# Performance work log

Hardware: AMD Instinct MI355X
Metric: run time of the kernel (lower is better)

## Reference

```python
import jax, jax.numpy as jnp
import numpy as np

N, E = 20000, 320000
CUR, HID, OUT, H = 256, 256, 64, 6  # cur_dim, hidden_dim, output_dim, gat heads


def setup_inputs() -> dict:
    key = jax.random.key(0)
    ks = jax.random.split(key, 16)
    p = lambda k, shape: jax.random.normal(k, shape, jnp.float32) * 0.05
    return dict(
        x=jax.random.normal(ks[0], (N, CUR), jnp.float32),
        edge_index=jax.random.randint(ks[1], (2, E), 0, N),
        edge_weight=jax.random.uniform(ks[2], (E,), jnp.float32),
        Wp=p(ks[3], (CUR, HID)), bp=p(ks[4], (HID,)),
        W_gat=p(ks[5], (HID, H * OUT)),
        att_src=p(ks[6], (H, OUT)), att_dst=p(ks[7], (H, OUT)),
        b_gat=p(ks[8], (H * OUT,)),
        W_gcn0=p(ks[9], (HID, OUT)), b_gcn0=p(ks[10], (OUT,)),
        W_gcn1=p(ks[11], (HID, OUT)), b_gcn1=p(ks[12], (OUT,)),
        W_arma_init=p(ks[13], (H * OUT, OUT)),
        W_arma_root=p(ks[14], (H * OUT, OUT)),
        b_arma=p(ks[15], (OUT,)),
    )


def _seg_sum(v, ids, n):
    return jax.ops.segment_sum(v, ids, num_segments=n)


def _gat(h, src, dst, W, a_s, a_d, b):
    # PyG GATConv: add self loops, per-edge attention, softmax over incoming edges.
    n = h.shape[0]
    loops = jnp.arange(n)
    s = jnp.concatenate([src, loops])
    d = jnp.concatenate([dst, loops])
    xw = (h @ W).reshape(n, H, OUT)               # [N,H,F]
    al = (xw * a_s).sum(-1)                       # [N,H] source term
    ar = (xw * a_d).sum(-1)                       # [N,H] target term
    e = jax.nn.leaky_relu(al[s] + ar[d], 0.2)     # [E',H]
    m = jax.ops.segment_max(e, d, num_segments=n)  # stable softmax per target
    pe = jnp.exp(e - m[d])
    alpha = pe / _seg_sum(pe, d, n)[d]
    out = _seg_sum(alpha[:, :, None] * xw[s], d, n)  # [N,H,F]
    return out.reshape(n, H * OUT) + b


def _gcn(h, src, dst, w, W, b):
    # PyG GCNConv: self loops (weight 1), symmetric D^-1/2 A D^-1/2 normalization.
    n = h.shape[0]
    loops = jnp.arange(n)
    s = jnp.concatenate([src, loops])
    d = jnp.concatenate([dst, loops])
    w2 = jnp.concatenate([w, jnp.ones((n,), h.dtype)])
    deg = _seg_sum(w2, d, n)
    dinv = jnp.where(deg > 0, jax.lax.rsqrt(deg), 0.0)
    norm = dinv[s] * w2 * dinv[d]
    xw = h @ W
    return _seg_sum(norm[:, None] * xw[s], d, n) + b


def _arma(h, src, dst, w, Wi, Wr, b):
    # PyG ARMAConv, num_stacks=1, num_layers=1, act=ReLU; gcn_norm WITHOUT self loops.
    n = h.shape[0]
    deg = _seg_sum(w, dst, n)
    dinv = jnp.where(deg > 0, jax.lax.rsqrt(deg), 0.0)
    norm = dinv[src] * w * dinv[dst]
    t = h @ Wi
    agg = _seg_sum(norm[:, None] * t[src], dst, n)
    return jax.nn.relu(agg + h @ Wr + b)


def reference(x, edge_index, edge_weight, Wp, bp, W_gat, att_src, att_dst, b_gat,
              W_gcn0, b_gcn0, W_gcn1, b_gcn1, W_arma_init, W_arma_root, b_arma):
    src, dst = edge_index[0], edge_index[1]
    h = x @ Wp + bp
    lrelu = lambda v: jax.nn.leaky_relu(v, 0.01)  # F.leaky_relu default slope
    h1 = lrelu(_gat(h, src, dst, W_gat, att_src, att_dst, b_gat))   # [N, 6*64]
    h2 = lrelu(_gcn(h, src, dst, edge_weight, W_gcn0, b_gcn0))       # [N, 64]
    h3 = lrelu(_gcn(h, src, dst, edge_weight, W_gcn1, b_gcn1))       # [N, 64]
    h4 = lrelu(_arma(h1, src, dst, edge_weight, W_arma_init, W_arma_root, b_arma))
    return jnp.tanh(jnp.concatenate([h1, h2, h3, h4], axis=1))      # [N, 576]
```

## Files before the change

### kernel.cpp

```cpp
#include <hip/hip_runtime.h>


#define NN 20000
#define EE 320000
#define GATD 384
#define NH 6
#define OUTD 64
#define ODIM 576

typedef __bf16 bf16_8 __attribute__((ext_vector_type(8)));
typedef float f32_4 __attribute__((ext_vector_type(4)));

__device__ __forceinline__ float lrelu(float x, float s) { return x > 0.f ? x : s * x; }

__device__ __forceinline__ float loadf(const void* p, size_t i, int f32) {
  return f32 ? ((const float*)p)[i] : (float)((const __bf16*)p)[i];
}

struct ProbeArgs {
  const void* ptr[15];
  int cnt[15];
  int flagidx[15];
  const int* ei;
};
__global__ void k_probe_all(ProbeArgs a, int* __restrict__ flags) {
  __shared__ int cnt;
  if (threadIdx.x == 0) cnt = 0;
  __syncthreads();
  int b = blockIdx.x;
  if (b < 15) {
    const unsigned short* u = (const unsigned short*)a.ptr[b];
    int m = a.cnt[b] < 2048 ? a.cnt[b] : 2048;
    int c = 0;
    for (int i = threadIdx.x; i < m; i += 256) {
      float v = __uint_as_float(((unsigned int)u[i]) << 16);
      if (!(fabsf(v) < 1e4f)) c++;
    }
    if (c) atomicAdd(&cnt, c);
    __syncthreads();
    if (threadIdx.x == 0) flags[a.flagidx[b]] = (cnt > m / 16) ? 1 : 0;
  } else {
    int c = 0;
    for (int i = threadIdx.x; i < 1024; i += 256)
      if (a.ei[2 * i + 1] != 0) c++;
    if (c) atomicAdd(&cnt, c);
    __syncthreads();
    if (threadIdx.x == 0) flags[16] = (cnt <= 2) ? 1 : 0;
  }
}

struct CvtSeg { const void* in; __bf16* out; int n; int flagidx; int blk0; };
struct CvtArgs { CvtSeg s[7]; };
__global__ void k_cvt_all(CvtArgs a, const int* __restrict__ flags) {
  int b = blockIdx.x;
  int k = 0;
  while (k + 1 < 7 && a.s[k + 1].blk0 <= b) k++;
  const CvtSeg sg = a.s[k];
  int i = (b - sg.blk0) * 256 + threadIdx.x;
  if (i >= sg.n) return;
  sg.out[i] = flags[sg.flagidx] ? (__bf16)((const float*)sg.in)[i] : ((const __bf16*)sg.in)[i];
}

struct TSeg { const void* in; __bf16* out; int R; int C; int flagidx; int blk0; };
struct TArgs { TSeg s[6]; };
__global__ void k_cvt_t_all(TArgs a, const int* __restrict__ flags) {
  __shared__ float t[32][33];
  int b = blockIdx.x;
  int k = 0;
  while (k + 1 < 6 && a.s[k + 1].blk0 <= b) k++;
  const TSeg sg = a.s[k];
  int f32 = flags[sg.flagidx];
  int tpx = (sg.C + 31) >> 5;
  int lt = b - sg.blk0;
  int c0 = (lt % tpx) * 32, r0 = (lt / tpx) * 32;
  int tid = threadIdx.x;
  for (int idx = tid; idx < 1024; idx += 256) {
    int r = idx >> 5, c = idx & 31;
    if (r0 + r < sg.R && c0 + c < sg.C)
      t[r][c] = loadf(sg.in, (size_t)(r0 + r) * sg.C + (c0 + c), f32);
  }
  __syncthreads();
  for (int idx = tid; idx < 1024; idx += 256) {
    int r = idx >> 5, c = idx & 31;
    if (c0 + r < sg.C && r0 + c < sg.R)
      sg.out[(size_t)(c0 + r) * sg.R + (r0 + c)] = (__bf16)t[c][r];
  }
}

__global__ void k_count(const int* __restrict__ ei, const void* __restrict__ ew,
                        const int* __restrict__ flags,
                        int* __restrict__ deg, float* __restrict__ wdeg) {
  int e = blockIdx.x * 256 + threadIdx.x;
  if (e >= EE) return;
  int sh = flags[16];
  int d = ei[(size_t)(EE + e) << sh];
  atomicAdd(&deg[d], 1);
  atomicAdd(&wdeg[d], loadf(ew, e, flags[2]));
}

__global__ void k_scan(const int* __restrict__ deg, int* __restrict__ rowstart) {
  __shared__ int ps[256];
  int t = threadIdx.x;
  const int per = (NN + 255) / 256;
  int lo = t * per, hi = min(NN, lo + per);
  if (lo > NN) lo = NN;
  int s = 0;
  for (int i = lo; i < hi; i++) s += deg[i];
  ps[t] = s;
  __syncthreads();
  if (t == 0) { int a = 0; for (int i = 0; i < 256; i++) { int v = ps[i]; ps[i] = a; a += v; } }
  __syncthreads();
  int a = ps[t];
  for (int i = lo; i < hi; i++) { rowstart[i] = a; a += deg[i]; }
  if (t == 255) rowstart[NN] = a;
}

__global__ void k_fill(const int* __restrict__ ei, const void* __restrict__ ew,
                       const int* __restrict__ flags, const int* __restrict__ rowstart,
                       int* __restrict__ cursor,
                       int* __restrict__ csr_src, float* __restrict__ csr_w) {
  int e = blockIdx.x * 256 + threadIdx.x;
  if (e >= EE) return;
  int sh = flags[16];
  int d = ei[(size_t)(EE + e) << sh];
  int s = ei[(size_t)e << sh];
  int pos = rowstart[d] + atomicAdd(&cursor[d], 1);
  csr_src[pos] = s;
  csr_w[pos] = loadf(ew, e, flags[2]);
}

__global__ void k_dinv(const float* __restrict__ wdeg, float* __restrict__ dg, float* __restrict__ da) {
  int i = blockIdx.x * 256 + threadIdx.x;
  if (i >= NN) return;
  float w = wdeg[i];
  dg[i] = rsqrtf(w + 1.0f);
  da[i] = w > 0.f ? rsqrtf(w) : 0.f;
}

template<bool HAS_BIAS>
__global__ __launch_bounds__(256) void gemm64(const void* __restrict__ A,
    const int* __restrict__ aflag, const __bf16* __restrict__ Bt,
    const __bf16* __restrict__ bias, __bf16* __restrict__ Cout,
    int M, int N, int K, int ldc) {
  __shared__ __bf16 Al[64][40];
  __shared__ __bf16 Bl[64][40];
  int a32 = *aflag;
  int tid = threadIdx.x;
  int w = tid >> 6, lane = tid & 63;
  int quad = lane >> 4, r = lane & 15;
  int row0 = blockIdx.x * 64, col0 = blockIdx.y * 64;
  f32_4 acc[4] = {};
  int srow = tid >> 2;
  int koff = (tid & 3) * 8;
  for (int kt = 0; kt < K; kt += 32) {
    int arow = row0 + srow;
    if (a32) {
      float4 a0 = {0.f, 0.f, 0.f, 0.f}, a1 = {0.f, 0.f, 0.f, 0.f};
      if (arow < M) {
        const float* ap = (const float*)A + (size_t)arow * K + kt + koff;
        a0 = *(const float4*)ap;
        a1 = *(const float4*)(ap + 4);
      }
      bf16_8 t;
      t[0] = (__bf16)a0.x; t[1] = (__bf16)a0.y; t[2] = (__bf16)a0.z; t[3] = (__bf16)a0.w;
      t[4] = (__bf16)a1.x; t[5] = (__bf16)a1.y; t[6] = (__bf16)a1.z; t[7] = (__bf16)a1.w;
      *(bf16_8*)(&Al[srow][koff]) = t;
    } else {
      float4 av = {0.f, 0.f, 0.f, 0.f};
      if (arow < M) av = *(const float4*)((const __bf16*)A + (size_t)arow * K + kt + koff);
      *(float4*)(&Al[srow][koff]) = av;
    }
    float4 bv = *(const float4*)(Bt + (size_t)(col0 + srow) * K + kt + koff);
    *(float4*)(&Bl[srow][koff]) = bv;
    __syncthreads();
    bf16_8 bfrag = *(const bf16_8*)(&Bl[w * 16 + r][quad * 8]);
#pragma unroll
    for (int mt = 0; mt < 4; mt++) {
      bf16_8 afrag = *(const bf16_8*)(&Al[mt * 16 + r][quad * 8]);
      acc[mt] = __builtin_amdgcn_mfma_f32_16x16x32_bf16(afrag, bfrag, acc[mt], 0, 0, 0);
    }
    __syncthreads();
  }
  int ccol = col0 + w * 16 + r;
  float bv = HAS_BIAS ? (float)bias[ccol] : 0.0f;
#pragma unroll
  for (int mt = 0; mt < 4; mt++) {
#pragma unroll
    for (int rr = 0; rr < 4; rr++) {
      int crow = row0 + mt * 16 + quad * 4 + rr;
      if (crow < M) Cout[(size_t)crow * ldc + ccol] = (__bf16)(acc[mt][rr] + bv);
    }
  }
}

__global__ void k_alar_w(const __bf16* __restrict__ xwb, const __bf16* __restrict__ as_,
                         const __bf16* __restrict__ ad_,
                         float* __restrict__ al, float* __restrict__ ar) {
  int p = blockIdx.x * 4 + (threadIdx.x >> 6);
  int lane = threadIdx.x & 63;
  if (p >= NN * NH) return;
  int i = p / NH, h = p - i * NH;
  float xv = (float)xwb[(size_t)i * GATD + h * OUTD + lane];
  float s1 = xv * (float)as_[h * OUTD + lane];
  float s2 = xv * (float)ad_[h * OUTD + lane];
  for (int off = 32; off; off >>= 1) { s1 += __shfl_xor(s1, off); s2 += __shfl_xor(s2, off); }
  if (lane == 0) { al[p] = s1; ar[p] = s2; }
}

__global__ __launch_bounds__(256) void k_gat2(const __bf16* __restrict__ xwb,
    const float* __restrict__ al, const float* __restrict__ ar,
    const int* __restrict__ rowstart, const int* __restrict__ csr_src,
    const __bf16* __restrict__ bgat,
    __bf16* __restrict__ h1b, float* __restrict__ out) {
  int wv = threadIdx.x >> 6, lane = threadIdx.x & 63;
  int i = blockIdx.x * 4 + wv;
  __shared__ int   src_sh[4][64];
  __shared__ float ex_sh[4][64][NH];
  __shared__ int   mc_sh[4];
  int e0 = rowstart[i], e1 = rowstart[i + 1];
  if (lane == 0) mc_sh[wv] = (e1 - e0 + 63) >> 6;
  float arv[NH], exs[NH], acc[NH], denp[NH];
#pragma unroll
  for (int h = 0; h < NH; h++) arv[h] = ar[i * NH + h];
#pragma unroll
  for (int h = 0; h < NH; h++) {
    float e = lrelu(al[i * NH + h] + arv[h], 0.2f);
    exs[h] = __expf(e);
    acc[h] = exs[h] * (float)xwb[(size_t)i * GATD + h * OUTD + lane];
    denp[h] = 0.f;
  }
  __syncthreads();
  int mch = max(max(mc_sh[0], mc_sh[1]), max(mc_sh[2], mc_sh[3]));
  for (int c = 0; c < mch; c++) {
    if (c) __syncthreads();
    int base = e0 + c * 64;
    int cnt = e1 - base; cnt = cnt < 0 ? 0 : (cnt > 64 ? 64 : cnt);
    if (lane < cnt) {
      int s = csr_src[base + lane];
      src_sh[wv][lane] = s;
#pragma unroll
      for (int h = 0; h < NH; h++) {
        float ex = __expf(lrelu(al[s * NH + h] + arv[h], 0.2f));
        ex_sh[wv][lane][h] = ex;
        denp[h] += ex;
      }
    }
    __syncthreads();
    int j = 0;
    for (; j + 2 <= cnt; j += 2) {
      int s0 = src_sh[wv][j], s1 = src_sh[wv][j + 1];
      const __bf16* r0 = xwb + (size_t)s0 * GATD + lane;
      const __bf16* r1 = xwb + (size_t)s1 * GATD + lane;
      float x0[NH], x1[NH];
#pragma unroll
      for (int h = 0; h < NH; h++) { x0[h] = (float)r0[h * OUTD]; x1[h] = (float)r1[h * OUTD]; }
#pragma unroll
      for (int h = 0; h < NH; h++)
        acc[h] += ex_sh[wv][j][h] * x0[h] + ex_sh[wv][j + 1][h] * x1[h];
    }
    if (j < cnt) {
      int s0 = src_sh[wv][j];
      const __bf16* r0 = xwb + (size_t)s0 * GATD + lane;
#pragma unroll
      for (int h = 0; h < NH; h++) acc[h] += ex_sh[wv][j][h] * (float)r0[h * OUTD];
    }
  }
#pragma unroll
  for (int h = 0; h < NH; h++) {
    float d = denp[h];
    for (int off = 32; off; off >>= 1) d += __shfl_xor(d, off);
    d += exs[h];
    float v = acc[h] / d + (float)bgat[h * OUTD + lane];
    v = lrelu(v, 0.01f);
    h1b[(size_t)i * GATD + h * OUTD + lane] = (__bf16)v;
    out[(size_t)i * ODIM + h * OUTD + lane] = tanhf(v);
  }
}

__global__ __launch_bounds__(256) void k_gcnarma2(const __bf16* __restrict__ xwgb,
    const __bf16* __restrict__ trb, const int* __restrict__ rowstart,
    const int* __restrict__ csr_src, const float* __restrict__ csr_w,
    const float* __restrict__ dgcn, const float* __restrict__ darma,
    const __bf16* __restrict__ b0, const __bf16* __restrict__ b1,
    const __bf16* __restrict__ ba, float* __restrict__ out) {
  int wv = threadIdx.x >> 6, lane = threadIdx.x & 63;
  int i = blockIdx.x * 4 + wv;
  __shared__ int   src_sh[4][64];
  __shared__ float wg_sh[4][64], wa_sh[4][64];
  __shared__ int   mc_sh[4];
  int e0 = rowstart[i], e1 = rowstart[i + 1];
  if (lane == 0) mc_sh[wv] = (e1 - e0 + 63) >> 6;
  __syncthreads();
  int mch = max(max(mc_sh[0], mc_sh[1]), max(mc_sh[2], mc_sh[3]));
  float g0 = 0.f, g1 = 0.f, aa = 0.f;
  for (int c = 0; c < mch; c++) {
    if (c) __syncthreads();
    int base = e0 + c * 64;
    int cnt = e1 - base; cnt = cnt < 0 ? 0 : (cnt > 64 ? 64 : cnt);
    if (lane < cnt) {
      int eidx = base + lane;
      int s = csr_src[eidx];
      float wvv = csr_w[eidx];
      src_sh[wv][lane] = s;
      wg_sh[wv][lane] = dgcn[s] * wvv;
      wa_sh[wv][lane] = darma[s] * wvv;
    }
    __syncthreads();
    int j = 0;
    for (; j + 2 <= cnt; j += 2) {
      int s0 = src_sh[wv][j], s1 = src_sh[wv][j + 1];
      float wg0 = wg_sh[wv][j], wg1 = wg_sh[wv][j + 1];
      float wa0 = wa_sh[wv][j], wa1 = wa_sh[wv][j + 1];
      const __bf16* p0 = xwgb + (size_t)s0 * 128;
      const __bf16* p1 = xwgb + (size_t)s1 * 128;
      const __bf16* q0 = trb + (size_t)s0 * 128;
      const __bf16* q1 = trb + (size_t)s1 * 128;
      g0 += wg0 * (float)p0[lane] + wg1 * (float)p1[lane];
      g1 += wg0 * (float)p0[lane + 64] + wg1 * (float)p1[lane + 64];
      aa += wa0 * (float)q0[lane] + wa1 * (float)q1[lane];
    }
    if (j < cnt) {
      int s0 = src_sh[wv][j];
      float wg0 = wg_sh[wv][j], wa0 = wa_sh[wv][j];
      const __bf16* p0 = xwgb + (size_t)s0 * 128;
      const __bf16* q0 = trb + (size_t)s0 * 128;
      g0 += wg0 * (float)p0[lane];
      g1 += wg0 * (float)p0[lane + 64];
      aa += wa0 * (float)q0[lane];
    }
  }
  float di = dgcn[i];
  float v0 = lrelu(di * g0 + di * di * (float)xwgb[(size_t)i * 128 + lane] + (float)b0[lane], 0.01f);
  float v1 = lrelu(di * g1 + di * di * (float)xwgb[(size_t)i * 128 + 64 + lane] + (float)b1[lane], 0.01f);
  out[(size_t)i * ODIM + 384 + lane] = tanhf(v0);
  out[(size_t)i * ODIM + 448 + lane] = tanhf(v1);
  float va = darma[i] * aa + (float)trb[(size_t)i * 128 + 64 + lane] + (float)ba[lane];
  va = fmaxf(va, 0.f);
  out[(size_t)i * ODIM + 512 + lane] = tanhf(va);
}

extern "C" void kernel_launch(void* const* d_in, const int* in_sizes, int n_in,
                              void* d_out, int out_size, void* d_ws, size_t ws_size,
                              hipStream_t stream) {
  const int* ei = (const int*)d_in[1];
  float* out = (float*)d_out;

  char* ws = (char*)d_ws;
  size_t off = 0;
  auto alloc = [&](size_t bytes) -> void* {
    void* p = ws + off;
    off += (bytes + 255) & ~(size_t)255;
    return p;
  };
  int*    flags    = (int*)alloc(32 * 4);
  int*    deg      = (int*)alloc((size_t)3 * NN * 4);
  int*    cursor   = deg + NN;
  float*  wdeg     = (float*)(deg + 2 * NN);
  int*    rowstart = (int*)alloc((size_t)(NN + 1) * 4);
  int*    csr_src  = (int*)alloc((size_t)EE * 4);
  float*  csr_w    = (float*)alloc((size_t)EE * 4);
  float*  dgcn     = (float*)alloc((size_t)NN * 4);
  float*  darma    = (float*)alloc((size_t)NN * 4);
  float*  al       = (float*)alloc((size_t)NN * NH * 4);
  float*  ar       = (float*)alloc((size_t)NN * NH * 4);
  __bf16* bpb   = (__bf16*)alloc(256 * 2);
  __bf16* asb   = (__bf16*)alloc(384 * 2);
  __bf16* adb   = (__bf16*)alloc(384 * 2);
  __bf16* bgatb = (__bf16*)alloc(384 * 2);
  __bf16* bg0b  = (__bf16*)alloc(64 * 2);
  __bf16* bg1b  = (__bf16*)alloc(64 * 2);
  __bf16* bab   = (__bf16*)alloc(64 * 2);
  __bf16* Wp_t    = (__bf16*)alloc(256 * 256 * 2);
  __bf16* Wgat_t  = (__bf16*)alloc(384 * 256 * 2);
  __bf16* Wg01_t  = (__bf16*)alloc(128 * 256 * 2);
  __bf16* Warma_t = (__bf16*)alloc(128 * 384 * 2);
  char* regA = (char*)alloc((size_t)NN * GATD * 2);
  __bf16* h   = (__bf16*)regA;
  __bf16* h1b = (__bf16*)regA;
  char* regB = (char*)alloc((size_t)NN * GATD * 2);
  __bf16* xwb = (__bf16*)regB;
  __bf16* trb = (__bf16*)regB;
  __bf16* xwgb = (__bf16*)alloc((size_t)NN * 128 * 2);
  (void)ws_size; (void)in_sizes; (void)n_in; (void)out_size;

  hipMemsetAsync(ws, 0, 256 + (size_t)3 * NN * 4, stream);

  dim3 tb(256);
  ProbeArgs pa;
  const int pidx[15] = {0, 2, 3, 4, 5, 6, 7, 8, 9, 10, 11, 12, 13, 14, 15};
  const int pcnt[15] = {NN * 256, EE, 256 * 256, 256, 256 * 384, NH * OUTD, NH * OUTD,
                        NH * OUTD, 256 * 64, 64, 256 * 64, 64, GATD * OUTD, GATD * OUTD, 64};
  for (int k = 0; k < 15; k++) { pa.ptr[k] = d_in[pidx[k]]; pa.cnt[k] = pcnt[k]; pa.flagidx[k] = pidx[k]; }
  pa.ei = ei;
  k_probe_all<<<dim3(16), tb, 0, stream>>>(pa, flags);

  CvtArgs ca;
  {
    struct { int idx; __bf16* out; int n; } cv[7] = {
      {4, bpb, 256}, {6, asb, 384}, {7, adb, 384}, {8, bgatb, 384},
      {10, bg0b, 64}, {12, bg1b, 64}, {15, bab, 64},
    };
    int blk = 0;
    for (int k = 0; k < 7; k++) {
      ca.s[k].in = d_in[cv[k].idx]; ca.s[k].out = cv[k].out; ca.s[k].n = cv[k].n;
      ca.s[k].flagidx = cv[k].idx; ca.s[k].blk0 = blk;
      blk += (cv[k].n + 255) / 256;
    }
    k_cvt_all<<<dim3(blk), tb, 0, stream>>>(ca, flags);
  }

  TArgs ta;
  {
    struct { int idx; __bf16* out; int R; int C; } tv[6] = {
      {3,  Wp_t,             256, 256},
      {5,  Wgat_t,           256, 384},
      {9,  Wg01_t,           256, 64},
      {11, Wg01_t + 64 * 256, 256, 64},
      {13, Warma_t,          384, 64},
      {14, Warma_t + 64 * 384, 384, 64},
    };
    int blk = 0;
    for (int k = 0; k < 6; k++) {
      ta.s[k].in = d_in[tv[k].idx]; ta.s[k].out = tv[k].out;
      ta.s[k].R = tv[k].R; ta.s[k].C = tv[k].C;
      ta.s[k].flagidx = tv[k].idx; ta.s[k].blk0 = blk;
      blk += ((tv[k].R + 31) / 32) * ((tv[k].C + 31) / 32);
    }
    k_cvt_t_all<<<dim3(blk), tb, 0, stream>>>(ta, flags);
  }

  k_count<<<dim3((EE + 255) / 256), tb, 0, stream>>>(ei, d_in[2], flags, deg, wdeg);
  k_scan<<<dim3(1), tb, 0, stream>>>(deg, rowstart);
  k_fill<<<dim3((EE + 255) / 256), tb, 0, stream>>>(ei, d_in[2], flags, rowstart, cursor, csr_src, csr_w);
  k_dinv<<<dim3((NN + 255) / 256), tb, 0, stream>>>(wdeg, dgcn, darma);

  const int MB64 = (NN + 63) / 64;
  gemm64<true ><<<dim3(MB64, 4), tb, 0, stream>>>(d_in[0], &flags[0], Wp_t, bpb, h, NN, 256, 256, 256);
  gemm64<false><<<dim3(MB64, 6), tb, 0, stream>>>(h, &flags[30], Wgat_t, nullptr, xwb, NN, 384, 256, 384);
  k_alar_w<<<dim3((NN * NH + 3) / 4), tb, 0, stream>>>(xwb, asb, adb, al, ar);
  gemm64<false><<<dim3(MB64, 2), tb, 0, stream>>>(h, &flags[30], Wg01_t, nullptr, xwgb, NN, 128, 256, 128);
  k_gat2<<<dim3(NN / 4), tb, 0, stream>>>(xwb, al, ar, rowstart, csr_src, bgatb, h1b, out);
  gemm64<false><<<dim3(MB64, 2), tb, 0, stream>>>(h1b, &flags[30], Warma_t, nullptr, trb, NN, 128, 384, 128);
  k_gcnarma2<<<dim3(NN / 4), tb, 0, stream>>>(xwgb, trb, rowstart, csr_src, csr_w,
                                              dgcn, darma, bg0b, bg1b, bab, out);
}
```

Baseline: 342.6 us.

## Interleave head features in GEMM output and fuse GAT/GCN projection GEMMs

```diff
diff --git a/kernel.cpp b/kernel.cpp
--- a/kernel.cpp
+++ b/kernel.cpp
@@ -11,7 +11,11 @@
 typedef __bf16 bf16_8 __attribute__((ext_vector_type(8)));
 typedef float f32_4 __attribute__((ext_vector_type(4)));
 
+struct u96 { unsigned x, y, z; };
+
 __device__ __forceinline__ float lrelu(float x, float s) { return x > 0.f ? x : s * x; }
+__device__ __forceinline__ float bflo(unsigned p) { return __uint_as_float(p << 16); }
+__device__ __forceinline__ float bfhi(unsigned p) { return __uint_as_float(p & 0xffff0000u); }
 
 __device__ __forceinline__ float loadf(const void* p, size_t i, int f32) {
   return f32 ? ((const float*)p)[i] : (float)((const __bf16*)p)[i];
@@ -98,19 +102,26 @@
   atomicAdd(&wdeg[d], loadf(ew, e, flags[2]));
 }
 
-__global__ void k_scan(const int* __restrict__ deg, int* __restrict__ rowstart) {
-  __shared__ int ps[256];
+__global__ __launch_bounds__(256) void k_scan(const int* __restrict__ deg, int* __restrict__ rowstart) {
+  __shared__ int wsum[4];
   int t = threadIdx.x;
   const int per = (NN + 255) / 256;
-  int lo = t * per, hi = min(NN, lo + per);
-  if (lo > NN) lo = NN;
+  int lo = t * per; if (lo > NN) lo = NN;
+  int hi = lo + per; if (hi > NN) hi = NN;
   int s = 0;
   for (int i = lo; i < hi; i++) s += deg[i];
-  ps[t] = s;
+  int lane = t & 63, wv = t >> 6;
+  int run = s;
+  for (int off = 1; off < 64; off <<= 1) {
+    int u = __shfl_up(run, off);
+    if (lane >= off) run += u;
+  }
+  if (lane == 63) wsum[wv] = run;
   __syncthreads();
-  if (t == 0) { int a = 0; for (int i = 0; i < 256; i++) { int v = ps[i]; ps[i] = a; a += v; } }
-  __syncthreads();
-  int a = ps[t];
+  int wbase = 0;
+#pragma unroll
+  for (int w = 0; w < 4; w++) { int v = wsum[w]; if (w < wv) wbase += v; }
+  int a = wbase + run - s;
   for (int i = lo; i < hi; i++) { rowstart[i] = a; a += deg[i]; }
   if (t == 255) rowstart[NN] = a;
 }
@@ -140,8 +151,10 @@
 template<bool HAS_BIAS>
 __global__ __launch_bounds__(256) void gemm64(const void* __restrict__ A,
     const int* __restrict__ aflag, const __bf16* __restrict__ Bt,
-    const __bf16* __restrict__ bias, __bf16* __restrict__ Cout,
-    int M, int N, int K, int ldc) {
+    const __bf16* __restrict__ bias,
+    __bf16* __restrict__ C1, int n1, int ldc1, int P1,
+    __bf16* __restrict__ C2, int ldc2, int P2,
+    int M, int K) {
   __shared__ __bf16 Al[64][40];
   __shared__ __bf16 Bl[64][40];
   int a32 = *aflag;
@@ -181,33 +194,40 @@
     }
     __syncthreads();
   }
-  int ccol = col0 + w * 16 + r;
-  float bv = HAS_BIAS ? (float)bias[ccol] : 0.0f;
+  int ccg = col0 + w * 16 + r;
+  __bf16* Cp; int ldc; int ccol; int P;
+  if (col0 < n1) { Cp = C1; ldc = ldc1; ccol = ccg; P = P1; }
+  else           { Cp = C2; ldc = ldc2; ccol = ccg - n1; P = P2; }
+  int cc = (P > 1) ? ((ccol & 63) * P + (ccol >> 6)) : ccol;
+  float bv = HAS_BIAS ? (float)bias[ccg] : 0.0f;
 #pragma unroll
   for (int mt = 0; mt < 4; mt++) {
 #pragma unroll
     for (int rr = 0; rr < 4; rr++) {
       int crow = row0 + mt * 16 + quad * 4 + rr;
-      if (crow < M) Cout[(size_t)crow * ldc + ccol] = (__bf16)(acc[mt][rr] + bv);
-    }
-  }
-}
-
-__global__ void k_alar_w(const __bf16* __restrict__ xwb, const __bf16* __restrict__ as_,
+      if (crow < M) Cp[(size_t)crow * ldc + cc] = (__bf16)(acc[mt][rr] + bv);
+    }
+  }
+}
+
+__global__ void k_alar_w(const __bf16* __restrict__ xwp, const __bf16* __restrict__ as_,
                          const __bf16* __restrict__ ad_,
                          float* __restrict__ al, float* __restrict__ ar) {
-  int p = blockIdx.x * 4 + (threadIdx.x >> 6);
+  int i = blockIdx.x * 4 + (threadIdx.x >> 6);
   int lane = threadIdx.x & 63;
-  if (p >= NN * NH) return;
-  int i = p / NH, h = p - i * NH;
-  float xv = (float)xwb[(size_t)i * GATD + h * OUTD + lane];
-  float s1 = xv * (float)as_[h * OUTD + lane];
-  float s2 = xv * (float)ad_[h * OUTD + lane];
-  for (int off = 32; off; off >>= 1) { s1 += __shfl_xor(s1, off); s2 += __shfl_xor(s2, off); }
-  if (lane == 0) { al[p] = s1; ar[p] = s2; }
-}
-
-__global__ __launch_bounds__(256) void k_gat2(const __bf16* __restrict__ xwb,
+  if (i >= NN) return;
+  u96 u = *(const u96*)(xwp + (size_t)i * GATD + lane * 6);
+  float v[NH] = {bflo(u.x), bfhi(u.x), bflo(u.y), bfhi(u.y), bflo(u.z), bfhi(u.z)};
+#pragma unroll
+  for (int h = 0; h < NH; h++) {
+    float s1 = v[h] * (float)as_[h * OUTD + lane];
+    float s2 = v[h] * (float)ad_[h * OUTD + lane];
+    for (int off = 32; off; off >>= 1) { s1 += __shfl_xor(s1, off); s2 += __shfl_xor(s2, off); }
+    if (lane == 0) { al[i * NH + h] = s1; ar[i * NH + h] = s2; }
+  }
+}
+
+__global__ __launch_bounds__(256) void k_gat2(const __bf16* __restrict__ xwp,
     const float* __restrict__ al, const float* __restrict__ ar,
     const int* __restrict__ rowstart, const int* __restrict__ csr_src,
     const __bf16* __restrict__ bgat,
@@ -215,18 +235,20 @@
   int wv = threadIdx.x >> 6, lane = threadIdx.x & 63;
   int i = blockIdx.x * 4 + wv;
   __shared__ int   src_sh[4][64];
-  __shared__ float ex_sh[4][64][NH];
+  __shared__ __attribute__((aligned(16))) float ex_sh[4][64][NH];
   __shared__ int   mc_sh[4];
   int e0 = rowstart[i], e1 = rowstart[i + 1];
   if (lane == 0) mc_sh[wv] = (e1 - e0 + 63) >> 6;
   float arv[NH], exs[NH], acc[NH], denp[NH];
 #pragma unroll
   for (int h = 0; h < NH; h++) arv[h] = ar[i * NH + h];
+  u96 us = *(const u96*)(xwp + (size_t)i * GATD + lane * 6);
+  float sv[NH] = {bflo(us.x), bfhi(us.x), bflo(us.y), bfhi(us.y), bflo(us.z), bfhi(us.z)};
 #pragma unroll
   for (int h = 0; h < NH; h++) {
     float e = lrelu(al[i * NH + h] + arv[h], 0.2f);
     exs[h] = __expf(e);
-    acc[h] = exs[h] * (float)xwb[(size_t)i * GATD + h * OUTD + lane];
+    acc[h] = exs[h] * sv[h];
     denp[h] = 0.f;
   }
   __syncthreads();
@@ -248,21 +270,31 @@
     __syncthreads();
     int j = 0;
     for (; j + 2 <= cnt; j += 2) {
-      int s0 = src_sh[wv][j], s1 = src_sh[wv][j + 1];
-      const __bf16* r0 = xwb + (size_t)s0 * GATD + lane;
-      const __bf16* r1 = xwb + (size_t)s1 * GATD + lane;
-      float x0[NH], x1[NH];
-#pragma unroll
-      for (int h = 0; h < NH; h++) { x0[h] = (float)r0[h * OUTD]; x1[h] = (float)r1[h * OUTD]; }
-#pragma unroll
-      for (int h = 0; h < NH; h++)
-        acc[h] += ex_sh[wv][j][h] * x0[h] + ex_sh[wv][j + 1][h] * x1[h];
+      int2 ss = *(const int2*)&src_sh[wv][j];
+      u96 u0 = *(const u96*)(xwp + (size_t)ss.x * GATD + lane * 6);
+      u96 u1 = *(const u96*)(xwp + (size_t)ss.y * GATD + lane * 6);
+      const float2* ep0 = (const float2*)ex_sh[wv][j];
+      const float2* ep1 = (const float2*)ex_sh[wv][j + 1];
+      float2 ea0 = ep0[0], eb0 = ep0[1], ec0 = ep0[2];
+      float2 ea1 = ep1[0], eb1 = ep1[1], ec1 = ep1[2];
+      acc[0] += ea0.x * bflo(u0.x) + ea1.x * bflo(u1.x);
+      acc[1] += ea0.y * bfhi(u0.x) + ea1.y * bfhi(u1.x);
+      acc[2] += eb0.x * bflo(u0.y) + eb1.x * bflo(u1.y);
+      acc[3] += eb0.y * bfhi(u0.y) + eb1.y * bfhi(u1.y);
+      acc[4] += ec0.x * bflo(u0.z) + ec1.x * bflo(u1.z);
+      acc[5] += ec0.y * bfhi(u0.z) + ec1.y * bfhi(u1.z);
     }
     if (j < cnt) {
       int s0 = src_sh[wv][j];
-      const __bf16* r0 = xwb + (size_t)s0 * GATD + lane;
-#pragma unroll
-      for (int h = 0; h < NH; h++) acc[h] += ex_sh[wv][j][h] * (float)r0[h * OUTD];
+      u96 u0 = *(const u96*)(xwp + (size_t)s0 * GATD + lane * 6);
+      const float2* ep0 = (const float2*)ex_sh[wv][j];
+      float2 ea0 = ep0[0], eb0 = ep0[1], ec0 = ep0[2];
+      acc[0] += ea0.x * bflo(u0.x);
+      acc[1] += ea0.y * bfhi(u0.x);
+      acc[2] += eb0.x * bflo(u0.y);
+      acc[3] += eb0.y * bfhi(u0.y);
+      acc[4] += ec0.x * bflo(u0.z);
+      acc[5] += ec0.y * bfhi(u0.z);
     }
   }
 #pragma unroll
@@ -277,7 +309,7 @@
   }
 }
 
-__global__ __launch_bounds__(256) void k_gcnarma2(const __bf16* __restrict__ xwgb,
+__global__ __launch_bounds__(256) void k_gcnarma2(const __bf16* __restrict__ xwgp,
     const __bf16* __restrict__ trb, const int* __restrict__ rowstart,
     const int* __restrict__ csr_src, const float* __restrict__ csr_w,
     const float* __restrict__ dgcn, const float* __restrict__ darma,
@@ -286,7 +318,7 @@
   int wv = threadIdx.x >> 6, lane = threadIdx.x & 63;
   int i = blockIdx.x * 4 + wv;
   __shared__ int   src_sh[4][64];
-  __shared__ float wg_sh[4][64], wa_sh[4][64];
+  __shared__ __attribute__((aligned(16))) float wg_sh[4][64], wa_sh[4][64];
   __shared__ int   mc_sh[4];
   int e0 = rowstart[i], e1 = rowstart[i + 1];
   if (lane == 0) mc_sh[wv] = (e1 - e0 + 63) >> 6;
@@ -308,30 +340,31 @@
     __syncthreads();
     int j = 0;
     for (; j + 2 <= cnt; j += 2) {
-      int s0 = src_sh[wv][j], s1 = src_sh[wv][j + 1];
-      float wg0 = wg_sh[wv][j], wg1 = wg_sh[wv][j + 1];
-      float wa0 = wa_sh[wv][j], wa1 = wa_sh[wv][j + 1];
-      const __bf16* p0 = xwgb + (size_t)s0 * 128;
-      const __bf16* p1 = xwgb + (size_t)s1 * 128;
-      const __bf16* q0 = trb + (size_t)s0 * 128;
-      const __bf16* q1 = trb + (size_t)s1 * 128;
-      g0 += wg0 * (float)p0[lane] + wg1 * (float)p1[lane];
-      g1 += wg0 * (float)p0[lane + 64] + wg1 * (float)p1[lane + 64];
-      aa += wa0 * (float)q0[lane] + wa1 * (float)q1[lane];
+      int2 ss = *(const int2*)&src_sh[wv][j];
+      float2 wg = *(const float2*)&wg_sh[wv][j];
+      float2 wa = *(const float2*)&wa_sh[wv][j];
+      unsigned x0 = *(const unsigned*)(xwgp + (size_t)ss.x * 128 + lane * 2);
+      unsigned x1 = *(const unsigned*)(xwgp + (size_t)ss.y * 128 + lane * 2);
+      float t0 = (float)trb[(size_t)ss.x * 128 + lane];
+      float t1 = (float)trb[(size_t)ss.y * 128 + lane];
+      g0 += wg.x * bflo(x0) + wg.y * bflo(x1);
+      g1 += wg.x * bfhi(x0) + wg.y * bfhi(x1);
+      aa += wa.x * t0 + wa.y * t1;
     }
     if (j < cnt) {
       int s0 = src_sh[wv][j];
-      float wg0 = wg_sh[wv][j], wa0 = wa_sh[wv][j];
-      const __bf16* p0 = xwgb + (size_t)s0 * 128;
-      const __bf16* q0 = trb + (size_t)s0 * 128;
-      g0 += wg0 * (float)p0[lane];
-      g1 += wg0 * (float)p0[lane + 64];
-      aa += wa0 * (float)q0[lane];
+      float wgx = wg_sh[wv][j], wax = wa_sh[wv][j];
+      unsigned x0 = *(const unsigned*)(xwgp + (size_t)s0 * 128 + lane * 2);
+      float t0 = (float)trb[(size_t)s0 * 128 + lane];
+      g0 += wgx * bflo(x0);
+      g1 += wgx * bfhi(x0);
+      aa += wax * t0;
     }
   }
   float di = dgcn[i];
-  float v0 = lrelu(di * g0 + di * di * (float)xwgb[(size_t)i * 128 + lane] + (float)b0[lane], 0.01f);
-  float v1 = lrelu(di * g1 + di * di * (float)xwgb[(size_t)i * 128 + 64 + lane] + (float)b1[lane], 0.01f);
+  unsigned xs = *(const unsigned*)(xwgp + (size_t)i * 128 + lane * 2);
+  float v0 = lrelu(di * g0 + di * di * bflo(xs) + (float)b0[lane], 0.01f);
+  float v1 = lrelu(di * g1 + di * di * bfhi(xs) + (float)b1[lane], 0.01f);
   out[(size_t)i * ODIM + 384 + lane] = tanhf(v0);
   out[(size_t)i * ODIM + 448 + lane] = tanhf(v1);
   float va = darma[i] * aa + (float)trb[(size_t)i * 128 + 64 + lane] + (float)ba[lane];
@@ -371,16 +404,17 @@
   __bf16* bg1b  = (__bf16*)alloc(64 * 2);
   __bf16* bab   = (__bf16*)alloc(64 * 2);
   __bf16* Wp_t    = (__bf16*)alloc(256 * 256 * 2);
-  __bf16* Wgat_t  = (__bf16*)alloc(384 * 256 * 2);
-  __bf16* Wg01_t  = (__bf16*)alloc(128 * 256 * 2);
+  __bf16* Wcat_t  = (__bf16*)alloc((size_t)(384 + 128) * 256 * 2);
+  __bf16* Wgat_t  = Wcat_t;
+  __bf16* Wg01_t  = Wcat_t + (size_t)384 * 256;
   __bf16* Warma_t = (__bf16*)alloc(128 * 384 * 2);
   char* regA = (char*)alloc((size_t)NN * GATD * 2);
   __bf16* h   = (__bf16*)regA;
   __bf16* h1b = (__bf16*)regA;
   char* regB = (char*)alloc((size_t)NN * GATD * 2);
-  __bf16* xwb = (__bf16*)regB;
+  __bf16* xwp = (__bf16*)regB;
   __bf16* trb = (__bf16*)regB;
-  __bf16* xwgb = (__bf16*)alloc((size_t)NN * 128 * 2);
+  __bf16* xwgp = (__bf16*)alloc((size_t)NN * 128 * 2);
   (void)ws_size; (void)in_sizes; (void)n_in; (void)out_size;
 
   hipMemsetAsync(ws, 0, 256 + (size_t)3 * NN * 4, stream);
@@ -435,12 +469,14 @@
   k_dinv<<<dim3((NN + 255) / 256), tb, 0, stream>>>(wdeg, dgcn, darma);
 
   const int MB64 = (NN + 63) / 64;
-  gemm64<true ><<<dim3(MB64, 4), tb, 0, stream>>>(d_in[0], &flags[0], Wp_t, bpb, h, NN, 256, 256, 256);
-  gemm64<false><<<dim3(MB64, 6), tb, 0, stream>>>(h, &flags[30], Wgat_t, nullptr, xwb, NN, 384, 256, 384);
-  k_alar_w<<<dim3((NN * NH + 3) / 4), tb, 0, stream>>>(xwb, asb, adb, al, ar);
-  gemm64<false><<<dim3(MB64, 2), tb, 0, stream>>>(h, &flags[30], Wg01_t, nullptr, xwgb, NN, 128, 256, 128);
-  k_gat2<<<dim3(NN / 4), tb, 0, stream>>>(xwb, al, ar, rowstart, csr_src, bgatb, h1b, out);
-  gemm64<false><<<dim3(MB64, 2), tb, 0, stream>>>(h1b, &flags[30], Warma_t, nullptr, trb, NN, 128, 384, 128);
-  k_gcnarma2<<<dim3(NN / 4), tb, 0, stream>>>(xwgb, trb, rowstart, csr_src, csr_w,
+  gemm64<true ><<<dim3(MB64, 4), tb, 0, stream>>>(d_in[0], &flags[0], Wp_t, bpb,
+                                                  h, 256, 256, 1, nullptr, 0, 1, NN, 256);
+  gemm64<false><<<dim3(MB64, 8), tb, 0, stream>>>(h, &flags[30], Wcat_t, nullptr,
+                                                  xwp, 384, 384, 6, xwgp, 128, 2, NN, 256);
+  k_alar_w<<<dim3(NN / 4), tb, 0, stream>>>(xwp, asb, adb, al, ar);
+  k_gat2<<<dim3(NN / 4), tb, 0, stream>>>(xwp, al, ar, rowstart, csr_src, bgatb, h1b, out);
+  gemm64<false><<<dim3(MB64, 2), tb, 0, stream>>>(h1b, &flags[30], Warma_t, nullptr,
+                                                  trb, 128, 128, 1, nullptr, 0, 1, NN, 384);
+  k_gcnarma2<<<dim3(NN / 4), tb, 0, stream>>>(xwgp, trb, rowstart, csr_src, csr_w,
                                               dgcn, darma, bg0b, bg1b, bab, out);
 }
```

Measured after the change: 349.5 us. +2.0%, slower.

## Widen GEMM tiles to 128 columns, fuse GAT/GCN projections, warp-shuffle scan

Applied to the files above, without the earlier changes.

```diff
diff --git a/kernel.cpp b/kernel.cpp
--- a/kernel.cpp
+++ b/kernel.cpp
@@ -98,19 +98,26 @@
   atomicAdd(&wdeg[d], loadf(ew, e, flags[2]));
 }
 
-__global__ void k_scan(const int* __restrict__ deg, int* __restrict__ rowstart) {
-  __shared__ int ps[256];
+__global__ __launch_bounds__(256) void k_scan(const int* __restrict__ deg, int* __restrict__ rowstart) {
+  __shared__ int wsum[4];
   int t = threadIdx.x;
   const int per = (NN + 255) / 256;
-  int lo = t * per, hi = min(NN, lo + per);
-  if (lo > NN) lo = NN;
+  int lo = t * per; if (lo > NN) lo = NN;
+  int hi = lo + per; if (hi > NN) hi = NN;
   int s = 0;
   for (int i = lo; i < hi; i++) s += deg[i];
-  ps[t] = s;
+  int lane = t & 63, wv = t >> 6;
+  int run = s;
+  for (int off = 1; off < 64; off <<= 1) {
+    int u = __shfl_up(run, off);
+    if (lane >= off) run += u;
+  }
+  if (lane == 63) wsum[wv] = run;
   __syncthreads();
-  if (t == 0) { int a = 0; for (int i = 0; i < 256; i++) { int v = ps[i]; ps[i] = a; a += v; } }
-  __syncthreads();
-  int a = ps[t];
+  int wbase = 0;
+#pragma unroll
+  for (int w = 0; w < 4; w++) { int v = wsum[w]; if (w < wv) wbase += v; }
+  int a = wbase + run - s;
   for (int i = lo; i < hi; i++) { rowstart[i] = a; a += deg[i]; }
   if (t == 255) rowstart[NN] = a;
 }
@@ -140,18 +147,22 @@
 template<bool HAS_BIAS>
 __global__ __launch_bounds__(256) void gemm64(const void* __restrict__ A,
     const int* __restrict__ aflag, const __bf16* __restrict__ Bt,
-    const __bf16* __restrict__ bias, __bf16* __restrict__ Cout,
-    int M, int N, int K, int ldc) {
+    const __bf16* __restrict__ bias,
+    __bf16* __restrict__ C1, int n1, int ldc1,
+    __bf16* __restrict__ C2, int ldc2,
+    int M, int K) {
   __shared__ __bf16 Al[64][40];
-  __shared__ __bf16 Bl[64][40];
+  __shared__ __bf16 Bl[128][40];
   int a32 = *aflag;
   int tid = threadIdx.x;
   int w = tid >> 6, lane = tid & 63;
   int quad = lane >> 4, r = lane & 15;
-  int row0 = blockIdx.x * 64, col0 = blockIdx.y * 64;
-  f32_4 acc[4] = {};
+  int row0 = blockIdx.x * 64, col0 = blockIdx.y * 128;
+  f32_4 acc[4][2] = {};
   int srow = tid >> 2;
   int koff = (tid & 3) * 8;
+  int brow = tid >> 1;
+  int bko  = (tid & 1) * 16;
   for (int kt = 0; kt < K; kt += 32) {
     int arow = row0 + srow;
     if (a32) {
@@ -170,25 +181,36 @@
       if (arow < M) av = *(const float4*)((const __bf16*)A + (size_t)arow * K + kt + koff);
       *(float4*)(&Al[srow][koff]) = av;
     }
-    float4 bv = *(const float4*)(Bt + (size_t)(col0 + srow) * K + kt + koff);
-    *(float4*)(&Bl[srow][koff]) = bv;
-    __syncthreads();
-    bf16_8 bfrag = *(const bf16_8*)(&Bl[w * 16 + r][quad * 8]);
+    const __bf16* bp = Bt + (size_t)(col0 + brow) * K + kt + bko;
+    *(float4*)(&Bl[brow][bko])     = *(const float4*)bp;
+    *(float4*)(&Bl[brow][bko + 8]) = *(const float4*)(bp + 8);
+    __syncthreads();
+    bf16_8 bfrag0 = *(const bf16_8*)(&Bl[w * 16 + r][quad * 8]);
+    bf16_8 bfrag1 = *(const bf16_8*)(&Bl[64 + w * 16 + r][quad * 8]);
 #pragma unroll
     for (int mt = 0; mt < 4; mt++) {
       bf16_8 afrag = *(const bf16_8*)(&Al[mt * 16 + r][quad * 8]);
-      acc[mt] = __builtin_amdgcn_mfma_f32_16x16x32_bf16(afrag, bfrag, acc[mt], 0, 0, 0);
-    }
-    __syncthreads();
-  }
-  int ccol = col0 + w * 16 + r;
-  float bv = HAS_BIAS ? (float)bias[ccol] : 0.0f;
+      acc[mt][0] = __builtin_amdgcn_mfma_f32_16x16x32_bf16(afrag, bfrag0, acc[mt][0], 0, 0, 0);
+      acc[mt][1] = __builtin_amdgcn_mfma_f32_16x16x32_bf16(afrag, bfrag1, acc[mt][1], 0, 0, 0);
+    }
+    __syncthreads();
+  }
+  __bf16* Cp; int ldc; int cbase;
+  if (col0 < n1) { Cp = C1; ldc = ldc1; cbase = col0; }
+  else           { Cp = C2; ldc = ldc2; cbase = col0 - n1; }
+  int cc0 = cbase + w * 16 + r;
+  int cc1 = cbase + 64 + w * 16 + r;
+  float bv0 = HAS_BIAS ? (float)bias[col0 + w * 16 + r] : 0.0f;
+  float bv1 = HAS_BIAS ? (float)bias[col0 + 64 + w * 16 + r] : 0.0f;
 #pragma unroll
   for (int mt = 0; mt < 4; mt++) {
 #pragma unroll
     for (int rr = 0; rr < 4; rr++) {
       int crow = row0 + mt * 16 + quad * 4 + rr;
-      if (crow < M) Cout[(size_t)crow * ldc + ccol] = (__bf16)(acc[mt][rr] + bv);
+      if (crow < M) {
+        Cp[(size_t)crow * ldc + cc0] = (__bf16)(acc[mt][0][rr] + bv0);
+        Cp[(size_t)crow * ldc + cc1] = (__bf16)(acc[mt][1][rr] + bv1);
+      }
     }
   }
 }
@@ -371,8 +393,9 @@
   __bf16* bg1b  = (__bf16*)alloc(64 * 2);
   __bf16* bab   = (__bf16*)alloc(64 * 2);
   __bf16* Wp_t    = (__bf16*)alloc(256 * 256 * 2);
-  __bf16* Wgat_t  = (__bf16*)alloc(384 * 256 * 2);
-  __bf16* Wg01_t  = (__bf16*)alloc(128 * 256 * 2);
+  __bf16* Wcat_t  = (__bf16*)alloc((size_t)(384 + 128) * 256 * 2);
+  __bf16* Wgat_t  = Wcat_t;
+  __bf16* Wg01_t  = Wcat_t + (size_t)384 * 256;
   __bf16* Warma_t = (__bf16*)alloc(128 * 384 * 2);
   char* regA = (char*)alloc((size_t)NN * GATD * 2);
   __bf16* h   = (__bf16*)regA;
@@ -435,12 +458,14 @@
   k_dinv<<<dim3((NN + 255) / 256), tb, 0, stream>>>(wdeg, dgcn, darma);
 
   const int MB64 = (NN + 63) / 64;
-  gemm64<true ><<<dim3(MB64, 4), tb, 0, stream>>>(d_in[0], &flags[0], Wp_t, bpb, h, NN, 256, 256, 256);
-  gemm64<false><<<dim3(MB64, 6), tb, 0, stream>>>(h, &flags[30], Wgat_t, nullptr, xwb, NN, 384, 256, 384);
+  gemm64<true ><<<dim3(MB64, 2), tb, 0, stream>>>(d_in[0], &flags[0], Wp_t, bpb,
+                                                  h, 256, 256, nullptr, 0, NN, 256);
+  gemm64<false><<<dim3(MB64, 4), tb, 0, stream>>>(h, &flags[30], Wcat_t, nullptr,
+                                                  xwb, 384, 384, xwgb, 128, NN, 256);
   k_alar_w<<<dim3((NN * NH + 3) / 4), tb, 0, stream>>>(xwb, asb, adb, al, ar);
-  gemm64<false><<<dim3(MB64, 2), tb, 0, stream>>>(h, &flags[30], Wg01_t, nullptr, xwgb, NN, 128, 256, 128);
   k_gat2<<<dim3(NN / 4), tb, 0, stream>>>(xwb, al, ar, rowstart, csr_src, bgatb, h1b, out);
-  gemm64<false><<<dim3(MB64, 2), tb, 0, stream>>>(h1b, &flags[30], Warma_t, nullptr, trb, NN, 128, 384, 128);
+  gemm64<false><<<dim3(MB64, 1), tb, 0, stream>>>(h1b, &flags[30], Warma_t, nullptr,
+                                                  trb, 128, 128, nullptr, 0, NN, 384);
   k_gcnarma2<<<dim3(NN / 4), tb, 0, stream>>>(xwgb, trb, rowstart, csr_src, csr_w,
                                               dgcn, darma, bg0b, bg1b, bab, out);
 }
```

After: 329.5 us. 1.04x faster.
